# Performance work log

Hardware: AMD Instinct MI355X
Metric: run time of the kernel (lower is better)

The kernel has to match this reference:

```python
import jax, jax.numpy as jnp
import numpy as np

K = 1024      # num_embeddings
D = 256       # embedding_dim
BETA = 0.25


def setup_inputs() -> dict:
    key = jax.random.key(0)
    k1, k2 = jax.random.split(key)
    z = jax.random.normal(k1, (4, D, 16, 32, 32), dtype=jnp.float32)
    # matches torch init: uniform(-1/K, 1/K)
    embedding = jax.random.uniform(k2, (K, D), dtype=jnp.float32,
                                   minval=-1.0 / K, maxval=1.0 / K)
    return {"z": z, "embedding": embedding}


def reference(z, embedding):
    # z: (B, C, Dd, H, W) with C == D
    z_perm = jnp.transpose(z, (0, 2, 3, 4, 1))          # (B, Dd, H, W, C)
    flat = z_perm.reshape(-1, D)                        # (N, D)

    dist = (jnp.sum(flat * flat, axis=1, keepdims=True)
            + jnp.sum(embedding * embedding, axis=1)
            - 2.0 * flat @ embedding.T)
    indices_flat = jnp.argmin(dist, axis=1)             # (N,)

    # one-hot @ embedding == direct gather
    z_q_flat = embedding[indices_flat]                  # (N, D)
    z_q = z_q_flat.reshape(z_perm.shape)

    commitment_loss = jnp.mean((z_perm - jax.lax.stop_gradient(z_q)) ** 2)
    vq_loss = BETA * commitment_loss

    # straight-through estimator
    z_q_st = z_perm + jax.lax.stop_gradient(z_q - z_perm)
    z_q_out = jnp.transpose(z_q_st, (0, 4, 1, 2, 3))    # back to (B, C, Dd, H, W)

    # perplexity from assignment histogram
    n = flat.shape[0]
    counts = jnp.zeros((K,), dtype=flat.dtype).at[indices_flat].add(1.0)
    avg_probs = counts / n
    perplexity = jnp.exp(-jnp.sum(avg_probs * jnp.log(avg_probs + 1e-10)))

    indices = indices_flat.reshape(z_perm.shape[:-1])   # (B, Dd, H, W)
    return z_q_out, vq_loss, indices, perplexity
```

## Files before the change

kernel.cpp:

```cpp
#include <hip/hip_runtime.h>

#define Dd 256
#define Kc 1024
#define SPATIAL 16384
#define NROWS 65536
#define NELEM 16777216
#define LOSS_OFF 16777216
#define IDX_OFF  16777217
#define PERP_OFF (16777217 + 65536)
#define MARGIN 3.5e-4f

typedef _Float16 f16x8 __attribute__((ext_vector_type(8)));
typedef _Float16 f16x2 __attribute__((ext_vector_type(2)));
typedef float f32x4 __attribute__((ext_vector_type(4)));


__global__ __launch_bounds__(256) void prep2_kernel(const float* __restrict__ emb,
                                                    _Float16* __restrict__ efp,
                                                    float* __restrict__ se) {
  const int j = blockIdx.x, c = threadIdx.x;
  float v = emb[j * Dd + c];
  const int ct2 = j >> 4, l15 = j & 15;
  const int kk = c >> 5, q = (c >> 3) & 3, e = c & 7;
  efp[((size_t)(ct2 * 8 + kk) * 64 + q * 16 + l15) * 8 + e] = (_Float16)(v * 1024.0f);
  double s = (double)v * (double)v;
  #pragma unroll
  for (int off = 32; off; off >>= 1) s += __shfl_down(s, off, 64);
  __shared__ double ws4[4];
  if ((threadIdx.x & 63) == 0) ws4[threadIdx.x >> 6] = s;
  __syncthreads();
  if (threadIdx.x == 0) se[j] = (float)(ws4[0] + ws4[1] + ws4[2] + ws4[3]);
}

__global__ __launch_bounds__(512, 4) void prefilter2_kernel(const float* __restrict__ z,
                                                            const _Float16* __restrict__ efp,
                                                            const float* __restrict__ se,
                                                            float* __restrict__ sx,
                                                            float* __restrict__ rowmin,
                                                            int* __restrict__ candcount,
                                                            int* __restrict__ cand_g) {
  __shared__ _Float16 As[32 * 272];
  __shared__ double sxp[16][32];
  __shared__ float selds[Kc];
  __shared__ int cnts[32];
  __shared__ int cands[32][8];
  __shared__ float rminw[8][32];
  __shared__ float rthr[32];

  const int tid = threadIdx.x;
  const int n0 = blockIdx.x * 32;
  const int b = n0 >> 14, s0 = n0 & 16383;
  const float* zb = z + (size_t)b * (Dd * SPATIAL) + s0;

  {
    const int r = tid & 31, cp = tid >> 5;
    double acc = 0.0;
    #pragma unroll
    for (int c = cp * 16; c < cp * 16 + 16; ++c) {
      const float v = zb[(size_t)c * SPATIAL + r];
      As[r * 272 + c] = (_Float16)v;
      acc += (double)v * (double)v;
    }
    sxp[cp][r] = acc;
  }
  selds[tid] = se[tid];
  selds[tid + 512] = se[tid + 512];
  if (tid < 32) cnts[tid] = 0;
  __syncthreads();
  if (tid < 32) {
    double s = 0.0;
    #pragma unroll
    for (int p = 0; p < 16; ++p) s += sxp[p][tid];
    sx[n0 + tid] = (float)s;
  }

  const int w = tid >> 6, lane = tid & 63, q = lane >> 4, l15 = lane & 15;
  const int colbase = w * 128;

  f16x8 Afrag[2][8];
  #pragma unroll
  for (int rt = 0; rt < 2; ++rt)
    #pragma unroll
    for (int kk = 0; kk < 8; ++kk)
      Afrag[rt][kk] = *(const f16x8*)(&As[(rt * 16 + l15) * 272 + kk * 32 + q * 8]);

  float rmin8[8];
  #pragma unroll
  for (int i = 0; i < 8; ++i) rmin8[i] = 3.4e38f;
  f16x2 scst[8][4];

  #pragma unroll
  for (int ct = 0; ct < 8; ++ct) {
    const _Float16* bp = efp + ((size_t)((w * 8 + ct) * 8) * 64 + lane) * 8;
    f32x4 a0 = {0.f, 0.f, 0.f, 0.f}, a1 = {0.f, 0.f, 0.f, 0.f};
    #pragma unroll
    for (int kk = 0; kk < 8; ++kk) {
      const f16x8 B = *(const f16x8*)(bp + kk * 512);
      a0 = __builtin_amdgcn_mfma_f32_16x16x32_f16(Afrag[0][kk], B, a0, 0, 0, 0);
      a1 = __builtin_amdgcn_mfma_f32_16x16x32_f16(Afrag[1][kk], B, a1, 0, 0, 0);
    }
    const float sec = selds[colbase + ct * 16 + l15];
    #pragma unroll
    for (int reg = 0; reg < 4; ++reg) {
      const float sc0 = fmaf(-0.001953125f, a0[reg], sec);
      const float sc1 = fmaf(-0.001953125f, a1[reg], sec);
      rmin8[reg]     = fminf(rmin8[reg], sc0);
      rmin8[reg + 4] = fminf(rmin8[reg + 4], sc1);
      scst[ct][reg] = (f16x2){(_Float16)sc0, (_Float16)sc1};
    }
  }

  #pragma unroll
  for (int m = 1; m <= 8; m <<= 1)
    #pragma unroll
    for (int i = 0; i < 8; ++i) rmin8[i] = fminf(rmin8[i], __shfl_xor(rmin8[i], m, 64));
  if (l15 == 0) {
    #pragma unroll
    for (int reg = 0; reg < 4; ++reg) {
      rminw[w][q * 4 + reg] = rmin8[reg];
      rminw[w][16 + q * 4 + reg] = rmin8[4 + reg];
    }
  }
  __syncthreads();
  if (tid < 32) {
    float m = rminw[0][tid];
    #pragma unroll
    for (int ww = 1; ww < 8; ++ww) m = fminf(m, rminw[ww][tid]);
    rowmin[n0 + tid] = m;
    rthr[tid] = m + MARGIN;
  }
  __syncthreads();

  float thr0[4], thr1[4];
  #pragma unroll
  for (int reg = 0; reg < 4; ++reg) {
    thr0[reg] = rthr[q * 4 + reg];
    thr1[reg] = rthr[16 + q * 4 + reg];
  }
  #pragma unroll
  for (int ct = 0; ct < 8; ++ct) {
    const int col = colbase + ct * 16 + l15;
    #pragma unroll
    for (int reg = 0; reg < 4; ++reg) {
      if ((float)scst[ct][reg][0] < thr0[reg]) {
        const int pos = atomicAdd(&cnts[q * 4 + reg], 1);
        if (pos < 8) cands[q * 4 + reg][pos] = col;
      }
      if ((float)scst[ct][reg][1] < thr1[reg]) {
        const int pos = atomicAdd(&cnts[16 + q * 4 + reg], 1);
        if (pos < 8) cands[16 + q * 4 + reg][pos] = col;
      }
    }
  }
  __syncthreads();
  if (tid < 32) candcount[n0 + tid] = cnts[tid];
  if (tid < 256)
    cand_g[(size_t)(n0 + (tid >> 3)) * 8 + (tid & 7)] = cands[tid >> 3][tid & 7];
}

__global__ __launch_bounds__(256) void resolve_easy_kernel(const int* __restrict__ candcount,
                                                           const int* __restrict__ cand_g,
                                                           const float* __restrict__ sx,
                                                           const float* __restrict__ rowmin,
                                                           float* __restrict__ out_idx_f,
                                                           int* __restrict__ idx_i,
                                                           int* __restrict__ counts,
                                                           int* __restrict__ hardcnt,
                                                           int* __restrict__ hardlist,
                                                           double* __restrict__ loss_sum) {
  const int tid = threadIdx.x;
  const int n = blockIdx.x * 256 + tid;
  const int cnt = candcount[n];
  double lp = 0.0;
  if (cnt == 1) {
    const int j = cand_g[(size_t)n * 8];
    idx_i[n] = j;
    out_idx_f[n] = (float)j;
    atomicAdd(&counts[j], 1);
    lp = (double)sx[n] + (double)rowmin[n];
  } else {
    const int pos = atomicAdd(hardcnt, 1);
    hardlist[pos] = n;
  }
  #pragma unroll
  for (int off = 32; off; off >>= 1) lp += __shfl_down(lp, off, 64);
  __shared__ double dred[4];
  if ((tid & 63) == 0) dred[tid >> 6] = lp;
  __syncthreads();
  if (tid == 0) atomicAdd(loss_sum, dred[0] + dred[1] + dred[2] + dred[3]);
}

__global__ __launch_bounds__(256) void resolve_hard_kernel(const float* __restrict__ z,
                                                           const float* __restrict__ emb,
                                                           const float* __restrict__ se,
                                                           const float* __restrict__ sx,
                                                           const int* __restrict__ candcount,
                                                           const int* __restrict__ cand_g,
                                                           const int* __restrict__ hardcnt,
                                                           const int* __restrict__ hardlist,
                                                           float* __restrict__ out_idx_f,
                                                           int* __restrict__ idx_i,
                                                           int* __restrict__ counts,
                                                           double* __restrict__ loss_sum) {
  __shared__ float xs[4][256];
  const int tid = threadIdx.x, w = tid >> 6, lane = tid & 63;
  const int hc = *hardcnt;
  const int nw = gridDim.x * 4;
  double wloss = 0.0;
  for (int i = blockIdx.x * 4 + w; i < hc; i += nw) {
    const int n = hardlist[i];
    const int b = n >> 14, s = n & 16383;
    #pragma unroll
    for (int ro = 0; ro < 4; ++ro)
      xs[w][ro * 64 + lane] =
          z[(size_t)b * (Dd * SPATIAL) + (size_t)(ro * 64 + lane) * SPATIAL + s];
    asm volatile("s_waitcnt lgkmcnt(0) vmcnt(0)" ::: "memory");
    const int cnt = candcount[n];
    const float sxn = sx[n];
    float scb = 3.4e38f;
    int jb = 0x7fffffff;
    if (cnt <= 8) {
      if (lane < cnt) {
        jb = cand_g[(size_t)n * 8 + lane];
        const float4* ep = (const float4*)(emb + (size_t)jb * Dd);
        float acc = 0.f;
        #pragma unroll 8
        for (int kk = 0; kk < 64; ++kk) {
          const float4 e4 = ep[kk];
          const float* xp = &xs[w][kk * 4];
          acc = fmaf(xp[0], e4.x, acc);
          acc = fmaf(xp[1], e4.y, acc);
          acc = fmaf(xp[2], e4.z, acc);
          acc = fmaf(xp[3], e4.w, acc);
        }
        const float t1 = sxn + se[jb];
        scb = t1 - 2.0f * acc;
      }
    } else {
      for (int jj = 0; jj < 16; ++jj) {
        const int j = lane * 16 + jj;
        const float4* ep = (const float4*)(emb + (size_t)j * Dd);
        float acc = 0.f;
        #pragma unroll 8
        for (int kk = 0; kk < 64; ++kk) {
          const float4 e4 = ep[kk];
          const float* xp = &xs[w][kk * 4];
          acc = fmaf(xp[0], e4.x, acc);
          acc = fmaf(xp[1], e4.y, acc);
          acc = fmaf(xp[2], e4.z, acc);
          acc = fmaf(xp[3], e4.w, acc);
        }
        const float t1 = sxn + se[j];
        const float sc = t1 - 2.0f * acc;
        if (sc < scb) { scb = sc; jb = j; }
      }
    }
    #pragma unroll
    for (int m = 1; m <= 32; m <<= 1) {
      const float so = __shfl_xor(scb, m, 64);
      const int jo = __shfl_xor(jb, m, 64);
      if (so < scb || (so == scb && jo < jb)) { scb = so; jb = jo; }
    }
    if (lane == 0) {
      idx_i[n] = jb;
      out_idx_f[n] = (float)jb;
      atomicAdd(&counts[jb], 1);
      wloss += (double)sxn + (double)scb;
    }
  }
  if (lane == 0) atomicAdd(loss_sum, wloss);
}

__global__ __launch_bounds__(256) void phase2c_kernel(const float* __restrict__ emb,
                                                      const int* __restrict__ idx_i,
                                                      float* __restrict__ out_zq) {
  __shared__ float els[64 * 257];
  __shared__ int sidx[64];
  const int tid = threadIdx.x;
  const int blk = blockIdx.x, b = blk >> 8, s0 = (blk & 255) << 6;
  if (tid < 64) sidx[tid] = idx_i[b * SPATIAL + s0 + tid];
  __syncthreads();
  {
    const int rr = tid >> 2, p = tid & 3;
    const float* ep = emb + (size_t)sidx[rr] * Dd + p * 64;
    float* dl = els + rr * 257 + p * 64;
    #pragma unroll
    for (int i = 0; i < 64; i += 4) {
      const float4 e4 = *(const float4*)(ep + i);
      dl[i] = e4.x; dl[i + 1] = e4.y; dl[i + 2] = e4.z; dl[i + 3] = e4.w;
    }
  }
  __syncthreads();
  const int s4 = tid & 15, cg = tid >> 4;
  const size_t zb = (size_t)b * (Dd * SPATIAL);
  #pragma unroll 4
  for (int c = cg; c < Dd; c += 16) {
    float4 v;
    v.x = els[(s4 * 4 + 0) * 257 + c];
    v.y = els[(s4 * 4 + 1) * 257 + c];
    v.z = els[(s4 * 4 + 2) * 257 + c];
    v.w = els[(s4 * 4 + 3) * 257 + c];
    *(float4*)(out_zq + zb + (size_t)c * SPATIAL + s0 + s4 * 4) = v;
  }
}

__global__ __launch_bounds__(256) void finalize_kernel(const int* __restrict__ counts,
                                                       const double* __restrict__ loss_sum,
                                                       float* __restrict__ out) {
  const int tid = threadIdx.x;
  double local = 0.0;
  for (int k = tid; k < Kc; k += 256) {
    const double p = (double)counts[k] / (double)NROWS;
    local += p * log(p + 1e-10);
  }
  #pragma unroll
  for (int off = 32; off; off >>= 1) local += __shfl_down(local, off, 64);
  __shared__ double dred[4];
  if ((tid & 63) == 0) dred[tid >> 6] = local;
  __syncthreads();
  if (tid == 0) {
    const double H = dred[0] + dred[1] + dred[2] + dred[3];
    out[PERP_OFF] = (float)exp(-H);
    out[LOSS_OFF] = (float)(0.25 * loss_sum[0] / (double)NELEM);
  }
}


__global__ __launch_bounds__(256) void prep_kernel(const float* __restrict__ emb,
                                                   float* __restrict__ eT,
                                                   float* __restrict__ se) {
  const int j = blockIdx.x, c = threadIdx.x;
  float v = emb[j * Dd + c];
  eT[c * Kc + j] = v;
  double s = (double)v * (double)v;
  #pragma unroll
  for (int off = 32; off; off >>= 1) s += __shfl_down(s, off, 64);
  __shared__ double ws4[4];
  if ((threadIdx.x & 63) == 0) ws4[threadIdx.x >> 6] = s;
  __syncthreads();
  if (threadIdx.x == 0) se[j] = (float)(ws4[0] + ws4[1] + ws4[2] + ws4[3]);
}

__global__ __launch_bounds__(256) void sx_kernel(const float* __restrict__ z,
                                                 float* __restrict__ sx) {
  __shared__ double part[4][64];
  const int tid = threadIdx.x, r = tid & 63, cg = tid >> 6;
  const int blk = blockIdx.x, b = blk >> 8, s0 = (blk & 255) << 6;
  const float* zb = z + (size_t)b * (Dd * SPATIAL);
  double acc = 0.0;
  for (int c = cg * 64; c < cg * 64 + 64; ++c) {
    const float v = zb[(size_t)c * SPATIAL + s0 + r];
    acc += (double)v * (double)v;
  }
  part[cg][r] = acc;
  __syncthreads();
  if (tid < 64)
    sx[b * SPATIAL + s0 + tid] =
        (float)(part[0][tid] + part[1][tid] + part[2][tid] + part[3][tid]);
}

__global__ __launch_bounds__(256) void argmin_kernel(const float* __restrict__ z,
                                                     const float* __restrict__ eT,
                                                     const float* __restrict__ se,
                                                     const float* __restrict__ sx,
                                                     float* __restrict__ out_idx_f,
                                                     int* __restrict__ idx_i,
                                                     int* __restrict__ counts) {
  __shared__ float As[32 * 64];
  __shared__ float Bs[32 * 64];
  __shared__ float ses[Kc];
  __shared__ float sxs[64];
  __shared__ float redS1[64 * 16];
  __shared__ int   redI1[64 * 16];
  const int tid = threadIdx.x, tc = tid & 15, tr = tid >> 4;
  const int blk = blockIdx.x, b = blk >> 8, s0 = (blk & 255) << 6;
  const float* zb = z + (size_t)b * (Dd * SPATIAL);
  #pragma unroll
  for (int i = 0; i < 4; ++i) ses[tid + 256 * i] = se[tid + 256 * i];
  if (tid < 64) sxs[tid] = sx[b * SPATIAL + s0 + tid];
  float s1[4]; int j1[4];
  #pragma unroll
  for (int r = 0; r < 4; ++r) { s1[r] = 3.4e38f; j1[r] = 0; }
  for (int j0 = 0; j0 < Kc; j0 += 64) {
    float acc[4][4];
    #pragma unroll
    for (int rr = 0; rr < 4; ++rr)
      #pragma unroll
      for (int cc = 0; cc < 4; ++cc) acc[rr][cc] = 0.0f;
    for (int c0 = 0; c0 < Dd; c0 += 32) {
      __syncthreads();
      #pragma unroll
      for (int i = 0; i < 8; ++i) {
        const int e = i * 256 + tid, ci = e >> 6, r = e & 63;
        As[e] = zb[(size_t)(c0 + ci) * SPATIAL + s0 + r];
        Bs[e] = eT[(c0 + ci) * Kc + j0 + r];
      }
      __syncthreads();
      #pragma unroll
      for (int d = 0; d < 32; ++d) {
        const float4 av = *reinterpret_cast<const float4*>(&As[d * 64 + 4 * tr]);
        const float4 bv = *reinterpret_cast<const float4*>(&Bs[d * 64 + 4 * tc]);
        const float aa[4] = {av.x, av.y, av.z, av.w};
        const float bb[4] = {bv.x, bv.y, bv.z, bv.w};
        #pragma unroll
        for (int rr = 0; rr < 4; ++rr)
          #pragma unroll
          for (int cc = 0; cc < 4; ++cc)
            acc[rr][cc] = fmaf(aa[rr], bb[cc], acc[rr][cc]);
      }
    }
    #pragma unroll
    for (int rr = 0; rr < 4; ++rr) {
      const float sxr = sxs[4 * tr + rr];
      #pragma unroll
      for (int cc = 0; cc < 4; ++cc) {
        const int j = j0 + 4 * tc + cc;
        const float t1 = sxr + ses[j];
        const float s = t1 - 2.0f * acc[rr][cc];
        if (s < s1[rr] || (s == s1[rr] && j < j1[rr])) { s1[rr] = s; j1[rr] = j; }
      }
    }
  }
  #pragma unroll
  for (int rr = 0; rr < 4; ++rr) {
    redS1[(4 * tr + rr) * 16 + tc] = s1[rr];
    redI1[(4 * tr + rr) * 16 + tc] = j1[rr];
  }
  __syncthreads();
  if (tid < 64) {
    float bs = redS1[tid * 16];
    int bj = redI1[tid * 16];
    #pragma unroll
    for (int t = 1; t < 16; ++t) {
      const float a1 = redS1[tid * 16 + t];
      const int aj = redI1[tid * 16 + t];
      if (a1 < bs || (a1 == bs && aj < bj)) { bs = a1; bj = aj; }
    }
    const int n = b * SPATIAL + s0 + tid;
    out_idx_f[n] = (float)bj;
    idx_i[n] = bj;
    atomicAdd(&counts[bj], 1);
  }
}

__global__ __launch_bounds__(256) void phase2_kernel(const float* __restrict__ z,
                                                     const float* __restrict__ eT,
                                                     const int* __restrict__ idx_i,
                                                     float* __restrict__ out_zq,
                                                     double* __restrict__ loss_sum) {
  __shared__ int sidx[64];
  __shared__ double dred[4];
  const int tid = threadIdx.x;
  const int blk = blockIdx.x, b = blk >> 8, s0 = (blk & 255) << 6;
  if (tid < 64) sidx[tid] = idx_i[b * SPATIAL + s0 + tid];
  __syncthreads();
  const int s = tid & 63, coff = tid >> 6;
  const size_t zb = (size_t)b * (Dd * SPATIAL);
  const int myidx = sidx[s];
  double lsum = 0.0;
  for (int c = coff; c < Dd; c += 4) {
    const size_t off = zb + (size_t)c * SPATIAL + s0 + s;
    const float zv = z[off];
    const float zq = eT[c * Kc + myidx];
    out_zq[off] = zv + (zq - zv);
    const float d = zv - zq;
    lsum += (double)d * (double)d;
  }
  #pragma unroll
  for (int off = 32; off; off >>= 1) lsum += __shfl_down(lsum, off, 64);
  if ((tid & 63) == 0) dred[tid >> 6] = lsum;
  __syncthreads();
  if (tid == 0) atomicAdd(loss_sum, dred[0] + dred[1] + dred[2] + dred[3]);
}


extern "C" void kernel_launch(void* const* d_in, const int* in_sizes, int n_in,
                              void* d_out, int out_size, void* d_ws, size_t ws_size,
                              hipStream_t stream) {
  const float* z   = (const float*)d_in[0];
  const float* emb = (const float*)d_in[1];
  float* out = (float*)d_out;
  char* ws = (char*)d_ws;

  const size_t OFF_SE   = 8192;
  const size_t OFF_SX   = 12288;
  const size_t OFF_EF   = 274432;
  const size_t OFF_RM   = 798720;
  const size_t OFF_IDX  = 1060864;
  const size_t OFF_CCT  = 1323008;
  const size_t OFF_CAND = 1585152;
  const size_t OFF_HARD = 3682304;
  const size_t NEED     = 3944448;

  double* loss_sum = (double*)(ws + 0);
  int*    hardcnt  = (int*)(ws + 8);
  int*    counts   = (int*)(ws + 256);

  hipMemsetAsync(d_ws, 0, 8192, stream);

  if (ws_size >= NEED) {
    float*    se        = (float*)(ws + OFF_SE);
    float*    sx        = (float*)(ws + OFF_SX);
    _Float16* efp       = (_Float16*)(ws + OFF_EF);
    float*    rowmin    = (float*)(ws + OFF_RM);
    int*      idx_i     = (int*)(ws + OFF_IDX);
    int*      candcount = (int*)(ws + OFF_CCT);
    int*      cand_g    = (int*)(ws + OFF_CAND);
    int*      hardlist  = (int*)(ws + OFF_HARD);

    prep2_kernel<<<Kc, 256, 0, stream>>>(emb, efp, se);
    prefilter2_kernel<<<2048, 512, 0, stream>>>(z, efp, se, sx, rowmin,
                                                candcount, cand_g);
    resolve_easy_kernel<<<256, 256, 0, stream>>>(candcount, cand_g, sx, rowmin,
                                                 out + IDX_OFF, idx_i, counts,
                                                 hardcnt, hardlist, loss_sum);
    resolve_hard_kernel<<<256, 256, 0, stream>>>(z, emb, se, sx, candcount, cand_g,
                                                 hardcnt, hardlist, out + IDX_OFF,
                                                 idx_i, counts, loss_sum);
    phase2c_kernel<<<1024, 256, 0, stream>>>(emb, idx_i, out);
    finalize_kernel<<<1, 256, 0, stream>>>(counts, loss_sum, out);
  } else {
    float* eT    = (float*)(ws + 8192);
    float* se    = (float*)(ws + 8192 + 1048576);
    float* sx    = (float*)(ws + 8192 + 1048576 + 4096);
    int*   idx_i = (int*)(ws + 8192 + 1048576 + 4096 + 262144);

    prep_kernel<<<Kc, 256, 0, stream>>>(emb, eT, se);
    sx_kernel<<<1024, 256, 0, stream>>>(z, sx);
    argmin_kernel<<<1024, 256, 0, stream>>>(z, eT, se, sx, out + IDX_OFF, idx_i, counts);
    phase2_kernel<<<1024, 256, 0, stream>>>(z, eT, idx_i, out, loss_sum);
    finalize_kernel<<<1, 256, 0, stream>>>(counts, loss_sum, out);
  }
}
```

Before: 287.9 us.

## Fuse easy-row resolution into prefilter and stage scores through shared memory

Folds the resolve_easy kernel into the prefilter kernel, so single-candidate rows write their index, histogram count and loss term directly. Hard rows are appended to the hard list with one wave-level ballot and a single atomic per block. The per-lane f16 score registers are replaced by a shared-memory score tile that reuses the A staging buffer. The candidate scan now reads that tile row-wise with vector loads. This removes a launch and the rowmin round trip through global memory, and lowers register pressure. In exchange, shared memory grows to about 67 KB per block, which may limit occupancy below the requested 4 blocks per CU.

```diff
diff --git a/kernel.cpp b/kernel.cpp
--- a/kernel.cpp
+++ b/kernel.cpp
@@ -9,9 +9,9 @@
 #define IDX_OFF  16777217
 #define PERP_OFF (16777217 + 65536)
 #define MARGIN 3.5e-4f
+#define SCSTRIDE 1048
 
 typedef _Float16 f16x8 __attribute__((ext_vector_type(8)));
-typedef _Float16 f16x2 __attribute__((ext_vector_type(2)));
 typedef float f32x4 __attribute__((ext_vector_type(4)));
 
 
@@ -36,10 +36,15 @@
                                                             const _Float16* __restrict__ efp,
                                                             const float* __restrict__ se,
                                                             float* __restrict__ sx,
-                                                            float* __restrict__ rowmin,
                                                             int* __restrict__ candcount,
-                                                            int* __restrict__ cand_g) {
-  __shared__ _Float16 As[32 * 272];
+                                                            int* __restrict__ cand_g,
+                                                            float* __restrict__ out_idx_f,
+                                                            int* __restrict__ idx_i,
+                                                            int* __restrict__ counts,
+                                                            int* __restrict__ hardcnt,
+                                                            int* __restrict__ hardlist,
+                                                            double* __restrict__ loss_sum) {
+  __shared__ __align__(16) _Float16 scAs[32 * SCSTRIDE];
   __shared__ double sxp[16][32];
   __shared__ float selds[Kc];
   __shared__ int cnts[32];
@@ -58,7 +63,7 @@
     #pragma unroll
     for (int c = cp * 16; c < cp * 16 + 16; ++c) {
       const float v = zb[(size_t)c * SPATIAL + r];
-      As[r * 272 + c] = (_Float16)v;
+      scAs[r * 272 + c] = (_Float16)v;
       acc += (double)v * (double)v;
     }
     sxp[cp][r] = acc;
@@ -67,11 +72,14 @@
   selds[tid + 512] = se[tid + 512];
   if (tid < 32) cnts[tid] = 0;
   __syncthreads();
+
+  float sxv = 0.0f;
   if (tid < 32) {
     double s = 0.0;
     #pragma unroll
     for (int p = 0; p < 16; ++p) s += sxp[p][tid];
-    sx[n0 + tid] = (float)s;
+    sxv = (float)s;
+    sx[n0 + tid] = sxv;
   }
 
   const int w = tid >> 6, lane = tid & 63, q = lane >> 4, l15 = lane & 15;
@@ -82,12 +90,13 @@
   for (int rt = 0; rt < 2; ++rt)
     #pragma unroll
     for (int kk = 0; kk < 8; ++kk)
-      Afrag[rt][kk] = *(const f16x8*)(&As[(rt * 16 + l15) * 272 + kk * 32 + q * 8]);
+      Afrag[rt][kk] = *(const f16x8*)(&scAs[(rt * 16 + l15) * 272 + kk * 32 + q * 8]);
+
+  __syncthreads();
 
   float rmin8[8];
   #pragma unroll
   for (int i = 0; i < 8; ++i) rmin8[i] = 3.4e38f;
-  f16x2 scst[8][4];
 
   #pragma unroll
   for (int ct = 0; ct < 8; ++ct) {
@@ -99,14 +108,16 @@
       a0 = __builtin_amdgcn_mfma_f32_16x16x32_f16(Afrag[0][kk], B, a0, 0, 0, 0);
       a1 = __builtin_amdgcn_mfma_f32_16x16x32_f16(Afrag[1][kk], B, a1, 0, 0, 0);
     }
-    const float sec = selds[colbase + ct * 16 + l15];
+    const int col = colbase + ct * 16 + l15;
+    const float sec = selds[col];
     #pragma unroll
     for (int reg = 0; reg < 4; ++reg) {
       const float sc0 = fmaf(-0.001953125f, a0[reg], sec);
       const float sc1 = fmaf(-0.001953125f, a1[reg], sec);
       rmin8[reg]     = fminf(rmin8[reg], sc0);
       rmin8[reg + 4] = fminf(rmin8[reg + 4], sc1);
-      scst[ct][reg] = (f16x2){(_Float16)sc0, (_Float16)sc1};
+      scAs[(q * 4 + reg) * SCSTRIDE + col]      = (_Float16)sc0;
+      scAs[(16 + q * 4 + reg) * SCSTRIDE + col] = (_Float16)sc1;
     }
   }
 
@@ -122,72 +133,66 @@
     }
   }
   __syncthreads();
+
+  float rm1 = 0.0f;
   if (tid < 32) {
     float m = rminw[0][tid];
     #pragma unroll
     for (int ww = 1; ww < 8; ++ww) m = fminf(m, rminw[ww][tid]);
-    rowmin[n0 + tid] = m;
+    rm1 = m;
     rthr[tid] = m + MARGIN;
   }
   __syncthreads();
 
-  float thr0[4], thr1[4];
-  #pragma unroll
-  for (int reg = 0; reg < 4; ++reg) {
-    thr0[reg] = rthr[q * 4 + reg];
-    thr1[reg] = rthr[16 + q * 4 + reg];
-  }
-  #pragma unroll
-  for (int ct = 0; ct < 8; ++ct) {
-    const int col = colbase + ct * 16 + l15;
-    #pragma unroll
-    for (int reg = 0; reg < 4; ++reg) {
-      if ((float)scst[ct][reg][0] < thr0[reg]) {
-        const int pos = atomicAdd(&cnts[q * 4 + reg], 1);
-        if (pos < 8) cands[q * 4 + reg][pos] = col;
-      }
-      if ((float)scst[ct][reg][1] < thr1[reg]) {
-        const int pos = atomicAdd(&cnts[16 + q * 4 + reg], 1);
-        if (pos < 8) cands[16 + q * 4 + reg][pos] = col;
-      }
-    }
-  }
-  __syncthreads();
-  if (tid < 32) candcount[n0 + tid] = cnts[tid];
+  {
+    const int row = tid >> 4, t4 = tid & 15;
+    const float thr = rthr[row];
+    #pragma unroll
+    for (int i = 0; i < 8; ++i) {
+      const f16x8 v = *(const f16x8*)(&scAs[row * SCSTRIDE + t4 * 8 + i * 128]);
+      #pragma unroll
+      for (int e = 0; e < 8; ++e) {
+        if ((float)v[e] < thr) {
+          const int pos = atomicAdd(&cnts[row], 1);
+          if (pos < 8) cands[row][pos] = t4 * 8 + i * 128 + e;
+        }
+      }
+    }
+  }
+  __syncthreads();
+
   if (tid < 256)
     cand_g[(size_t)(n0 + (tid >> 3)) * 8 + (tid & 7)] = cands[tid >> 3][tid & 7];
-}
-
-__global__ __launch_bounds__(256) void resolve_easy_kernel(const int* __restrict__ candcount,
-                                                           const int* __restrict__ cand_g,
-                                                           const float* __restrict__ sx,
-                                                           const float* __restrict__ rowmin,
-                                                           float* __restrict__ out_idx_f,
-                                                           int* __restrict__ idx_i,
-                                                           int* __restrict__ counts,
-                                                           int* __restrict__ hardcnt,
-                                                           int* __restrict__ hardlist,
-                                                           double* __restrict__ loss_sum) {
-  const int tid = threadIdx.x;
-  const int n = blockIdx.x * 256 + tid;
-  const int cnt = candcount[n];
-  double lp = 0.0;
-  if (cnt == 1) {
-    const int j = cand_g[(size_t)n * 8];
-    idx_i[n] = j;
-    out_idx_f[n] = (float)j;
-    atomicAdd(&counts[j], 1);
-    lp = (double)sx[n] + (double)rowmin[n];
-  } else {
-    const int pos = atomicAdd(hardcnt, 1);
-    hardlist[pos] = n;
-  }
-  #pragma unroll
-  for (int off = 32; off; off >>= 1) lp += __shfl_down(lp, off, 64);
-  __shared__ double dred[4];
-  if ((tid & 63) == 0) dred[tid >> 6] = lp;
-  __syncthreads();
-  if (tid == 0) atomicAdd(loss_sum, dred[0] + dred[1] + dred[2] + dred[3]);
+  if (tid < 64) {
+    double lp = 0.0;
+    int hard = 0;
+    const int n = n0 + tid;
+    if (tid < 32) {
+      const int cnt = cnts[tid];
+      candcount[n] = cnt;
+      if (cnt == 1) {
+        const int j = cands[tid][0];
+        idx_i[n] = j;
+        out_idx_f[n] = (float)j;
+        atomicAdd(&counts[j], 1);
+        lp = (double)sxv + (double)rm1;
+      } else {
+        hard = 1;
+      }
+    }
+    const unsigned long long mask = __ballot(hard);
+    const int h = __popcll(mask);
+    int base = 0;
+    if (tid == 0 && h) base = atomicAdd(hardcnt, h);
+    base = __shfl(base, 0, 64);
+    if (hard) {
+      const int rank = __popcll(mask & ((1ull << tid) - 1ull));
+      hardlist[base + rank] = n;
+    }
+    #pragma unroll
+    for (int off = 32; off; off >>= 1) lp += __shfl_down(lp, off, 64);
+    if (tid == 0 && lp != 0.0) atomicAdd(loss_sum, lp);
+  }
 }
 
 __global__ __launch_bounds__(256) void resolve_hard_kernel(const float* __restrict__ z,
@@ -491,6 +496,7 @@
   const size_t OFF_CAND = 1585152;
   const size_t OFF_HARD = 3682304;
   const size_t NEED     = 3944448;
+  (void)OFF_RM;
 
   double* loss_sum = (double*)(ws + 0);
   int*    hardcnt  = (int*)(ws + 8);
@@ -502,18 +508,15 @@
     float*    se        = (float*)(ws + OFF_SE);
     float*    sx        = (float*)(ws + OFF_SX);
     _Float16* efp       = (_Float16*)(ws + OFF_EF);
-    float*    rowmin    = (float*)(ws + OFF_RM);
     int*      idx_i     = (int*)(ws + OFF_IDX);
     int*      candcount = (int*)(ws + OFF_CCT);
     int*      cand_g    = (int*)(ws + OFF_CAND);
     int*      hardlist  = (int*)(ws + OFF_HARD);
 
     prep2_kernel<<<Kc, 256, 0, stream>>>(emb, efp, se);
-    prefilter2_kernel<<<2048, 512, 0, stream>>>(z, efp, se, sx, rowmin,
-                                                candcount, cand_g);
-    resolve_easy_kernel<<<256, 256, 0, stream>>>(candcount, cand_g, sx, rowmin,
-                                                 out + IDX_OFF, idx_i, counts,
-                                                 hardcnt, hardlist, loss_sum);
+    prefilter2_kernel<<<2048, 512, 0, stream>>>(z, efp, se, sx, candcount, cand_g,
+                                                out + IDX_OFF, idx_i, counts,
+                                                hardcnt, hardlist, loss_sum);
     resolve_hard_kernel<<<256, 256, 0, stream>>>(z, emb, se, sx, candcount, cand_g,
                                                  hardcnt, hardlist, out + IDX_OFF,
                                                  idx_i, counts, loss_sum);
```

Result: faster. 262.9 us (-8.7%).
